# Performance work log

Measured on AMD Instinct MI355X. Metric: run time of the kernel, lower is better.

## Reference

```python
import jax, jax.numpy as jnp
import numpy as np
import math

EPS = 1e-5

def _ln(x, g, b):
    m = jnp.mean(x, axis=-1, keepdims=True)
    v = jnp.mean((x - m) ** 2, axis=-1, keepdims=True)
    return (x - m) * jax.lax.rsqrt(v + EPS) * g + b

def _heads(t, H):
    B, T, C = t.shape
    return t.reshape(B, T, H, C // H).transpose(0, 2, 1, 3)  # [B,H,T,D]

def _merge(t):
    B, H, T, D = t.shape
    return t.transpose(0, 2, 1, 3).reshape(B, T, H * D)

def _self_attn(x, w, b, pw, pb, H):
    B, T, C = x.shape
    q, k, v = jnp.split(x @ w + b, 3, axis=-1)
    q, k, v = _heads(q, H), _heads(k, H), _heads(v, H)
    D = C // H
    att = jnp.einsum('bhqd,bhkd->bhqk', q, k) * (1.0 / math.sqrt(D))
    causal = jnp.tril(jnp.ones((T, T), bool))
    att = jnp.where(causal[None, None], att, jnp.float32(-jnp.inf))
    att = jax.nn.softmax(att, axis=-1)
    out = _merge(jnp.einsum('bhqk,bhkd->bhqd', att, v))
    return out @ pw + pb

def _cross_attn(enc, dec, w, b, pw, pb, H):
    B, Td, C = dec.shape
    q_dec = jnp.split(dec @ w + b, 3, axis=-1)[0]
    _, k_enc, v_enc = jnp.split(enc @ w + b, 3, axis=-1)
    q = _heads(q_dec, H); k = _heads(k_enc, H); v = _heads(v_enc, H)
    D = C // H
    att = jnp.einsum('bhqd,bhkd->bhqk', q, k) * (1.0 / math.sqrt(D))
    att = jax.nn.softmax(att, axis=-1)
    out = _merge(jnp.einsum('bhqk,bhkd->bhqd', att, v))
    return out @ pw + pb

def _block(x, encoder_embd,
           ln1_g, ln1_b, ln2_g, ln2_b, ln3_g, ln3_b,
           attn_w, attn_b, aproj_w, aproj_b,
           ca_w, ca_b, caproj_w, caproj_b,
           fc_w, fc_b, mproj_w, mproj_b,
           down_w, down_b, up_w, up_b, H=16):
    x = x + _self_attn(_ln(x, ln1_g, ln1_b), attn_w, attn_b, aproj_w, aproj_b, H)
    x = x + _cross_attn(encoder_embd, _ln(x, ln2_g, ln2_b), ca_w, ca_b, caproj_w, caproj_b, H)
    h = jax.nn.gelu(_ln(x, ln3_g, ln3_b) @ fc_w + fc_b, approximate=True) @ mproj_w + mproj_b
    adapt = jax.nn.gelu(h @ down_w + down_b, approximate=True) @ up_w + up_b + h  # Adapter residual
    return x + adapt


def setup_inputs() -> dict:
    key = jax.random.key(0)
    ks = jax.random.split(key, 12)
    B, T, Te, C, H = 4, 1024, 257, 1024, 16
    s = 0.02
    f32 = jnp.float32
    return {
        'x': jax.random.normal(ks[0], (B, T, C), f32),
        'encoder_embd': jax.random.normal(ks[1], (B, Te, C), f32),
        'prefix_embd': jnp.zeros((B, 1, C), f32),
        'ln1_g': jnp.ones((C,), f32), 'ln1_b': jnp.zeros((C,), f32),
        'ln2_g': jnp.ones((C,), f32), 'ln2_b': jnp.zeros((C,), f32),
        'ln3_g': jnp.ones((C,), f32), 'ln3_b': jnp.zeros((C,), f32),
        'attn_w': jax.random.normal(ks[2], (C, 3 * C), f32) * s,
        'attn_b': jnp.zeros((3 * C,), f32),
        'aproj_w': jax.random.normal(ks[3], (C, C), f32) * s,
        'aproj_b': jnp.zeros((C,), f32),
        'ca_w': jax.random.normal(ks[4], (C, 3 * C), f32) * s,
        'ca_b': jnp.zeros((3 * C,), f32),
        'caproj_w': jax.random.normal(ks[5], (C, C), f32) * s,
        'caproj_b': jnp.zeros((C,), f32),
        'fc_w': jax.random.normal(ks[6], (C, 4 * C), f32) * s,
        'fc_b': jnp.zeros((4 * C,), f32),
        'mproj_w': jax.random.normal(ks[7], (4 * C, C), f32) * s,
        'mproj_b': jnp.zeros((C,), f32),
        'down_w': jax.random.normal(ks[8], (C, C // 4), f32) * s,
        'down_b': jnp.zeros((C // 4,), f32),
        'up_w': jax.random.normal(ks[9], (C // 4, C), f32) * s,
        'up_b': jnp.zeros((C,), f32),
    }


def reference(x, encoder_embd, prefix_embd,
              ln1_g, ln1_b, ln2_g, ln2_b, ln3_g, ln3_b,
              attn_w, attn_b, aproj_w, aproj_b,
              ca_w, ca_b, caproj_w, caproj_b,
              fc_w, fc_b, mproj_w, mproj_b,
              down_w, down_b, up_w, up_b):
    # prefix_embd unused (peft='adapter')
    return _block(x, encoder_embd,
                  ln1_g, ln1_b, ln2_g, ln2_b, ln3_g, ln3_b,
                  attn_w, attn_b, aproj_w, aproj_b,
                  ca_w, ca_b, caproj_w, caproj_b,
                  fc_w, fc_b, mproj_w, mproj_b,
                  down_w, down_b, up_w, up_b)
```

## Files before the change

### kernel.cpp

```cpp
#include <hip/hip_runtime.h>

typedef __attribute__((ext_vector_type(8))) short short8v;
typedef __attribute__((ext_vector_type(8))) unsigned short ushort8v;
typedef __attribute__((ext_vector_type(4))) unsigned short ushort4v;
typedef __attribute__((ext_vector_type(4))) float f32x4;

__device__ __forceinline__ unsigned short f2b(float f) {
  unsigned int u = __float_as_uint(f);
  unsigned int r = (u + 0x7FFFu + ((u >> 16) & 1u)) >> 16;
  return (unsigned short)r;
}
__device__ __forceinline__ float b2f(unsigned short h) {
  return __uint_as_float(((unsigned int)h) << 16);
}
__device__ __forceinline__ float gelu_f(float x) {
  float z = 0.7978845608028654f * (x + 0.044715f * x * x * x);
  float e = __expf(2.0f * z);
  float t = 1.0f - 2.0f / (e + 1.0f);
  return 0.5f * x * (1.0f + t);
}
__device__ __forceinline__ void gload16(const void* g, void* l) {
  __builtin_amdgcn_global_load_lds((const __attribute__((address_space(1))) unsigned int*)g,
                                   (__attribute__((address_space(3))) unsigned int*)l,
                                   16, 0, 0);
}
__device__ __forceinline__ int xcd_swz(int wgid, int nwg) {
  int q = nwg >> 3, r = nwg & 7;
  int xcd = wgid & 7, idx = wgid >> 3;
  return (xcd < r ? xcd * (q + 1) : r * (q + 1) + (xcd - r) * q) + idx;
}

__global__ __launch_bounds__(256) void k_wprep(
    const float* aw, unsigned short* awt,
    const float* apw, unsigned short* apwt,
    const float* cw, unsigned short* cwt,
    const float* cpw, unsigned short* cpwt,
    const float* fw, unsigned short* fwt,
    const float* mw, unsigned short* mwt,
    const float* dw, unsigned short* dwt,
    const float* uw, unsigned short* uwt,
    const float* enc, unsigned short* encb) {
  __shared__ float tile[64][65];
  int bid = blockIdx.x, t = threadIdx.x;
  const float* w; unsigned short* wt; int K, N, gx, l;
  if      (bid < 768)  { w = aw;  wt = awt;  K = 1024; N = 3072; gx = 48; l = bid; }
  else if (bid < 1024) { w = apw; wt = apwt; K = 1024; N = 1024; gx = 16; l = bid - 768; }
  else if (bid < 1792) { w = cw;  wt = cwt;  K = 1024; N = 3072; gx = 48; l = bid - 1024; }
  else if (bid < 2048) { w = cpw; wt = cpwt; K = 1024; N = 1024; gx = 16; l = bid - 1792; }
  else if (bid < 3072) { w = fw;  wt = fwt;  K = 1024; N = 4096; gx = 64; l = bid - 2048; }
  else if (bid < 4096) { w = mw;  wt = mwt;  K = 4096; N = 1024; gx = 16; l = bid - 3072; }
  else if (bid < 4160) { w = dw;  wt = dwt;  K = 1024; N = 256;  gx = 4;  l = bid - 4096; }
  else if (bid < 4224) { w = uw;  wt = uwt;  K = 256;  N = 1024; gx = 16; l = bid - 4160; }
  else {
    size_t i = ((size_t)(bid - 4224) * 256 + t) * 4;
    f32x4 v = *(const f32x4*)&enc[i];
    ushort4v o;
#pragma unroll
    for (int j = 0; j < 4; ++j) o[j] = f2b(v[j]);
    *(ushort4v*)&encb[i] = o;
    return;
  }
  int bx = l % gx, by = l / gx;
  int tn = bx * 64, tk = by * 64;
  int c = t & 63, r0 = t >> 6;
#pragma unroll
  for (int p = 0; p < 16; ++p) {
    int r = r0 + p * 4;
    tile[r][c] = w[(size_t)(tk + r) * N + tn + c];
  }
  __syncthreads();
#pragma unroll
  for (int p = 0; p < 16; ++p) {
    int r = r0 + p * 4;
    wt[(size_t)(tn + r) * K + tk + c] = f2b(tile[c][r]);
  }
}

__global__ __launch_bounds__(256) void k_ln(const float* __restrict__ in,
                                            const float* __restrict__ g,
                                            const float* __restrict__ b,
                                            unsigned short* __restrict__ out) {
  int row = blockIdx.x;
  const float* x = in + (size_t)row * 1024;
  int t = threadIdx.x;
  float v0 = x[t], v1 = x[t + 256], v2 = x[t + 512], v3 = x[t + 768];
  float s = v0 + v1 + v2 + v3;
  float s2 = v0 * v0 + v1 * v1 + v2 * v2 + v3 * v3;
#pragma unroll
  for (int m = 1; m < 64; m <<= 1) { s += __shfl_xor(s, m); s2 += __shfl_xor(s2, m); }
  __shared__ float rs[4], rs2[4];
  int w = t >> 6;
  if ((t & 63) == 0) { rs[w] = s; rs2[w] = s2; }
  __syncthreads();
  s = rs[0] + rs[1] + rs[2] + rs[3];
  s2 = rs2[0] + rs2[1] + rs2[2] + rs2[3];
  float mean = s * (1.0f / 1024.0f);
  float var = s2 * (1.0f / 1024.0f) - mean * mean;
  float rinv = rsqrtf(var + 1e-5f);
  unsigned short* o = out + (size_t)row * 1024;
  o[t]       = f2b((v0 - mean) * rinv * g[t]       + b[t]);
  o[t + 256] = f2b((v1 - mean) * rinv * g[t + 256] + b[t + 256]);
  o[t + 512] = f2b((v2 - mean) * rinv * g[t + 512] + b[t + 512]);
  o[t + 768] = f2b((v3 - mean) * rinv * g[t + 768] + b[t + 768]);
}

template <bool GELU, bool WF32, bool WBF16, int NRES, bool RES1B>
__global__ __launch_bounds__(256) void k_gemm(
    const unsigned short* __restrict__ A, int lda,
    const unsigned short* __restrict__ W, int ldw,
    const float* __restrict__ bias,
    const float* __restrict__ res1, const unsigned short* __restrict__ res1b,
    const float* __restrict__ res2,
    float* __restrict__ outF, unsigned short* __restrict__ outB,
    int M, int N, int K, int nbx) {
  __shared__ unsigned short lds[16384];
  const int t = threadIdx.x;
  const int swz = xcd_swz(blockIdx.x, gridDim.x);
  const int tileM = (swz / nbx) * 128, tileN = (swz % nbx) * 128;
  const int lane = t & 63, w = t >> 6;
  const int wm = (w >> 1) * 64, wn = (w & 1) * 64;
  const int lr16 = lane & 15, kc4 = lane >> 4;

  const int row1 = t >> 2, row2 = (t >> 2) + 64, cs = t & 3;
  const int c1 = (cs ^ ((row1 >> 1) & 3)) * 8;
  const int c2 = (cs ^ ((row2 >> 1) & 3)) * 8;
  int gr1 = tileM + row1; if (gr1 >= M) gr1 = M - 1;
  int gr2 = tileM + row2; if (gr2 >= M) gr2 = M - 1;
  const unsigned short* a1 = A + (size_t)gr1 * lda + c1;
  const unsigned short* a2 = A + (size_t)gr2 * lda + c2;
  const unsigned short* w1 = W + (size_t)(tileN + row1) * ldw + c1;
  const unsigned short* w2 = W + (size_t)(tileN + row2) * ldw + c2;

  f32x4 acc[4][4];
#pragma unroll
  for (int i = 0; i < 4; ++i)
#pragma unroll
    for (int j = 0; j < 4; ++j) acc[i][j] = f32x4{0.f, 0.f, 0.f, 0.f};

  const int nsteps = K >> 5;
  for (int ks = 0; ks < nsteps; ++ks) {
    const int koff = ks << 5;
    gload16(a1 + koff, &lds[t * 8]);
    gload16(a2 + koff, &lds[2048 + t * 8]);
    gload16(w1 + koff, &lds[8192 + t * 8]);
    gload16(w2 + koff, &lds[10240 + t * 8]);
    __syncthreads();
    short8v af[4], bfr[4];
#pragma unroll
    for (int i = 0; i < 4; ++i) {
      int r = wm + i * 16 + lr16;
      af[i] = *(const short8v*)&lds[r * 32 + (kc4 ^ ((r >> 1) & 3)) * 8];
    }
#pragma unroll
    for (int j = 0; j < 4; ++j) {
      int r = wn + j * 16 + lr16;
      bfr[j] = *(const short8v*)&lds[8192 + r * 32 + (kc4 ^ ((r >> 1) & 3)) * 8];
    }
#pragma unroll
    for (int i = 0; i < 4; ++i)
#pragma unroll
      for (int j = 0; j < 4; ++j)
        acc[i][j] = __builtin_amdgcn_mfma_f32_16x16x32_bf16(af[i], bfr[j], acc[i][j], 0, 0, 0);
    __syncthreads();
  }

#pragma unroll
  for (int mi = 0; mi < 4; ++mi) {
#pragma unroll
    for (int n = 0; n < 4; ++n) {
      int col = tileN + wn + n * 16 + lr16;
      float bv = bias[col];
#pragma unroll
      for (int qi = 0; qi < 4; ++qi) {
        int row = tileM + wm + mi * 16 + kc4 * 4 + qi;
        if (row < M) {
          float v = acc[mi][n][qi] + bv;
          if (GELU) v = gelu_f(v);
          size_t o = (size_t)row * N + col;
          if (NRES >= 1) v += RES1B ? b2f(res1b[o]) : res1[o];
          if (NRES >= 2) v += res2[o];
          if (WF32) outF[o] = v;
          if (WBF16) outB[o] = f2b(v);
        }
      }
    }
  }
}

__global__ __launch_bounds__(256) void k_vtrans(const unsigned short* __restrict__ src,
                                                int src_stride, int src_off, int TB,
                                                unsigned short* __restrict__ dst, int dst_tstride) {
  __shared__ unsigned short tile[64][72];
  int tb = blockIdx.x, bh = blockIdx.y;
  int b = bh >> 4, h = bh & 15;
  int t = threadIdx.x;
  int r = t >> 2, c0 = (t & 3) * 16;
  int tok = tb * 64 + r; if (tok >= TB) tok = TB - 1;
  const unsigned short* s = src + (size_t)(b * TB + tok) * src_stride + src_off + h * 64 + c0;
  *(ushort8v*)&tile[r][c0] = *(const ushort8v*)s;
  *(ushort8v*)&tile[r][c0 + 8] = *(const ushort8v*)(s + 8);
  __syncthreads();
  unsigned short tmp[16];
#pragma unroll
  for (int j = 0; j < 16; ++j) tmp[j] = tile[c0 + j][r];
  unsigned short* dp = dst + ((size_t)bh * 64 + r) * dst_tstride + tb * 64 + c0;
  *(ushort8v*)dp = *(const ushort8v*)&tmp[0];
  *(ushort8v*)(dp + 8) = *(const ushort8v*)&tmp[8];
}

template <bool CAUSAL>
__global__ __launch_bounds__(256) void k_attn(
    const unsigned short* __restrict__ Qb, int q_stride,
    const unsigned short* __restrict__ Kb, int k_stride, int k_off, int TKR,
    const unsigned short* __restrict__ Vt, int vt_tstride,
    unsigned short* __restrict__ out, int Tk) {
  __shared__ unsigned short Kl[64 * 72];
  __shared__ unsigned short Vl[64 * 72];
  __shared__ unsigned short Pl[4][16 * 72];
  const int swz = xcd_swz(blockIdx.x, gridDim.x);
  int qb = swz & 15, bh = swz >> 4;
  int b = bh >> 4, h = bh & 15;
  int t = threadIdx.x, lane = t & 63, w = t >> 6;
  int g = lane >> 4, lc = lane & 15;

  int qrow_g = qb * 64 + w * 16 + lc;
  const unsigned short* qp = Qb + (size_t)(b * 1024 + qrow_g) * q_stride + h * 64 + g * 8;
  short8v aq0 = *(const short8v*)qp;
  short8v aq1 = *(const short8v*)(qp + 32);

  f32x4 o[4];
  float m_[4], l_[4];
#pragma unroll
  for (int dt = 0; dt < 4; ++dt) o[dt] = f32x4{0.f, 0.f, 0.f, 0.f};
#pragma unroll
  for (int r = 0; r < 4; ++r) { m_[r] = -3.0e38f; l_[r] = 0.0f; }

  int srow = t >> 2;
  int sc = (t & 3) * 16;
  int ntiles = CAUSAL ? (qb + 1) : ((Tk + 63) >> 6);

  for (int kt = 0; kt < ntiles; ++kt) {
    __syncthreads();
    {
      int kg = kt * 64 + srow;
      if (!CAUSAL && kg >= Tk) kg = Tk - 1;
      const unsigned short* ks = Kb + (size_t)(b * TKR + kg) * k_stride + k_off + h * 64 + sc;
      *(ushort8v*)&Kl[srow * 72 + sc]     = *(const ushort8v*)ks;
      *(ushort8v*)&Kl[srow * 72 + sc + 8] = *(const ushort8v*)(ks + 8);
      const unsigned short* vs = Vt + ((size_t)bh * 64 + srow) * vt_tstride + kt * 64 + sc;
      *(ushort8v*)&Vl[srow * 72 + sc]     = *(const ushort8v*)vs;
      *(ushort8v*)&Vl[srow * 72 + sc + 8] = *(const ushort8v*)(vs + 8);
    }
    __syncthreads();

    f32x4 s[4];
#pragma unroll
    for (int jt = 0; jt < 4; ++jt) {
      short8v bk0 = *(const short8v*)&Kl[(jt * 16 + lc) * 72 + g * 8];
      short8v bk1 = *(const short8v*)&Kl[(jt * 16 + lc) * 72 + g * 8 + 32];
      f32x4 acc = f32x4{0.f, 0.f, 0.f, 0.f};
      acc = __builtin_amdgcn_mfma_f32_16x16x32_bf16(aq0, bk0, acc, 0, 0, 0);
      acc = __builtin_amdgcn_mfma_f32_16x16x32_bf16(aq1, bk1, acc, 0, 0, 0);
      s[jt] = acc;
    }
#pragma unroll
    for (int jt = 0; jt < 4; ++jt)
#pragma unroll
      for (int r = 0; r < 4; ++r) {
        float sv = s[jt][r] * 0.125f;
        bool masked = CAUSAL ? (kt == qb && (jt * 16 + lc) > (w * 16 + g * 4 + r))
                             : (kt * 64 + jt * 16 + lc >= Tk);
        s[jt][r] = masked ? -3.0e38f : sv;
      }
    float f[4];
#pragma unroll
    for (int r = 0; r < 4; ++r) {
      float mx = fmaxf(fmaxf(s[0][r], s[1][r]), fmaxf(s[2][r], s[3][r]));
      mx = fmaxf(mx, __shfl_xor(mx, 1));
      mx = fmaxf(mx, __shfl_xor(mx, 2));
      mx = fmaxf(mx, __shfl_xor(mx, 4));
      mx = fmaxf(mx, __shfl_xor(mx, 8));
      float mnew = fmaxf(m_[r], mx);
      f[r] = __expf(m_[r] - mnew);
      m_[r] = mnew;
      float rsum = 0.0f;
#pragma unroll
      for (int jt = 0; jt < 4; ++jt) {
        float p = __expf(s[jt][r] - mnew);
        s[jt][r] = p;
        rsum += p;
      }
      rsum += __shfl_xor(rsum, 1);
      rsum += __shfl_xor(rsum, 2);
      rsum += __shfl_xor(rsum, 4);
      rsum += __shfl_xor(rsum, 8);
      l_[r] = l_[r] * f[r] + rsum;
    }
#pragma unroll
    for (int dt = 0; dt < 4; ++dt)
#pragma unroll
      for (int r = 0; r < 4; ++r) o[dt][r] *= f[r];
#pragma unroll
    for (int jt = 0; jt < 4; ++jt)
#pragma unroll
      for (int r = 0; r < 4; ++r)
        Pl[w][(g * 4 + r) * 72 + jt * 16 + lc] = f2b(s[jt][r]);
    short8v ap0 = *(const short8v*)&Pl[w][lc * 72 + g * 8];
    short8v ap1 = *(const short8v*)&Pl[w][lc * 72 + g * 8 + 32];
#pragma unroll
    for (int dt = 0; dt < 4; ++dt) {
      short8v bv0 = *(const short8v*)&Vl[(dt * 16 + lc) * 72 + g * 8];
      short8v bv1 = *(const short8v*)&Vl[(dt * 16 + lc) * 72 + g * 8 + 32];
      o[dt] = __builtin_amdgcn_mfma_f32_16x16x32_bf16(ap0, bv0, o[dt], 0, 0, 0);
      o[dt] = __builtin_amdgcn_mfma_f32_16x16x32_bf16(ap1, bv1, o[dt], 0, 0, 0);
    }
  }
  size_t orow = (size_t)(b * 1024 + qb * 64 + w * 16) * 1024 + h * 64;
#pragma unroll
  for (int r = 0; r < 4; ++r) {
    float inv = 1.0f / l_[r];
#pragma unroll
    for (int dt = 0; dt < 4; ++dt)
      out[orow + (size_t)(g * 4 + r) * 1024 + dt * 16 + lc] = f2b(o[dt][r] * inv);
  }
}

extern "C" void kernel_launch(void* const* d_in, const int* in_sizes, int n_in,
                              void* d_out, int out_size, void* d_ws, size_t ws_size,
                              hipStream_t stream) {
  (void)in_sizes; (void)n_in; (void)out_size; (void)ws_size;
  const float* x       = (const float*)d_in[0];
  const float* enc     = (const float*)d_in[1];
  const float* ln1_g   = (const float*)d_in[3];
  const float* ln1_b   = (const float*)d_in[4];
  const float* ln2_g   = (const float*)d_in[5];
  const float* ln2_b   = (const float*)d_in[6];
  const float* ln3_g   = (const float*)d_in[7];
  const float* ln3_b   = (const float*)d_in[8];
  const float* attn_w  = (const float*)d_in[9];
  const float* attn_b  = (const float*)d_in[10];
  const float* aproj_w = (const float*)d_in[11];
  const float* aproj_b = (const float*)d_in[12];
  const float* ca_w    = (const float*)d_in[13];
  const float* ca_b    = (const float*)d_in[14];
  const float* caproj_w= (const float*)d_in[15];
  const float* caproj_b= (const float*)d_in[16];
  const float* fc_w    = (const float*)d_in[17];
  const float* fc_b    = (const float*)d_in[18];
  const float* mproj_w = (const float*)d_in[19];
  const float* mproj_b = (const float*)d_in[20];
  const float* down_w  = (const float*)d_in[21];
  const float* down_b  = (const float*)d_in[22];
  const float* up_w    = (const float*)d_in[23];
  const float* up_b    = (const float*)d_in[24];
  float* out = (float*)d_out;
  char* ws = (char*)d_ws;

  const size_t O_WATTN = 0, O_WAPROJ = 6291456, O_WCA = 8388608, O_WCAPROJ = 14680064,
               O_WFC = 16777216, O_WMPROJ = 25165824, O_WDOWN = 33554432, O_WUP = 34078720,
               O_ENC = 34603008, O_LN = 36708352, O_BIG = 45096960,
               O_XRES = 78651392, O_ATTN = 112205824;

  unsigned short* wt_attn   = (unsigned short*)(ws + O_WATTN);
  unsigned short* wt_aproj  = (unsigned short*)(ws + O_WAPROJ);
  unsigned short* wt_ca     = (unsigned short*)(ws + O_WCA);
  unsigned short* wt_caproj = (unsigned short*)(ws + O_WCAPROJ);
  unsigned short* wt_fc     = (unsigned short*)(ws + O_WFC);
  unsigned short* wt_mproj  = (unsigned short*)(ws + O_WMPROJ);
  unsigned short* wt_down   = (unsigned short*)(ws + O_WDOWN);
  unsigned short* wt_up     = (unsigned short*)(ws + O_WUP);
  unsigned short* encbf     = (unsigned short*)(ws + O_ENC);
  unsigned short* lnout     = (unsigned short*)(ws + O_LN);
  unsigned short* hbf       = (unsigned short*)(ws + O_LN);
  unsigned short* qkvb      = (unsigned short*)(ws + O_BIG);
  unsigned short* vt_self   = (unsigned short*)(ws + O_BIG + 25165824);
  unsigned short* q2b       = (unsigned short*)(ws + O_BIG);
  unsigned short* kvb       = (unsigned short*)(ws + O_BIG + 8388608);
  unsigned short* vt_cross  = (unsigned short*)(ws + O_BIG + 12599296);
  unsigned short* caout     = (unsigned short*)(ws + O_BIG + 15220736);
  unsigned short* fcout     = (unsigned short*)(ws + O_BIG);
  float*          xres      = (float*)(ws + O_XRES);
  unsigned short* attnout   = (unsigned short*)(ws + O_ATTN);
  unsigned short* dmid      = (unsigned short*)(ws + O_ATTN);

  dim3 blk(256);

  k_wprep<<<dim3(5252), blk, 0, stream>>>(
      attn_w, wt_attn, aproj_w, wt_aproj, ca_w, wt_ca, caproj_w, wt_caproj,
      fc_w, wt_fc, mproj_w, wt_mproj, down_w, wt_down, up_w, wt_up, enc, encbf);

  k_ln<<<dim3(4096), blk, 0, stream>>>(x, ln1_g, ln1_b, lnout);
  k_gemm<false, false, true, 0, false><<<dim3(768), blk, 0, stream>>>(
      lnout, 1024, wt_attn, 1024, attn_b, nullptr, nullptr, nullptr, nullptr, qkvb,
      4096, 3072, 1024, 24);
  k_vtrans<<<dim3(16, 64), blk, 0, stream>>>(qkvb, 3072, 2048, 1024, vt_self, 1024);
  k_attn<true><<<dim3(1024), blk, 0, stream>>>(
      qkvb, 3072, qkvb, 3072, 1024, 1024, vt_self, 1024, attnout, 1024);
  k_gemm<false, true, false, 1, false><<<dim3(256), blk, 0, stream>>>(
      attnout, 1024, wt_aproj, 1024, aproj_b, x, nullptr, nullptr, xres, nullptr,
      4096, 1024, 1024, 8);

  k_ln<<<dim3(4096), blk, 0, stream>>>(xres, ln2_g, ln2_b, lnout);
  k_gemm<false, false, true, 0, false><<<dim3(256), blk, 0, stream>>>(
      lnout, 1024, wt_ca, 1024, ca_b, nullptr, nullptr, nullptr, nullptr, q2b,
      4096, 1024, 1024, 8);
  k_gemm<false, false, true, 0, false><<<dim3(144), blk, 0, stream>>>(
      encbf, 1024, wt_ca + (size_t)1024 * 1024, 1024, ca_b + 1024, nullptr, nullptr,
      nullptr, nullptr, kvb, 1028, 2048, 1024, 16);
  k_vtrans<<<dim3(5, 64), blk, 0, stream>>>(kvb, 2048, 1024, 257, vt_cross, 320);
  k_attn<false><<<dim3(1024), blk, 0, stream>>>(
      q2b, 1024, kvb, 2048, 0, 257, vt_cross, 320, caout, 257);
  k_gemm<false, true, false, 1, false><<<dim3(256), blk, 0, stream>>>(
      caout, 1024, wt_caproj, 1024, caproj_b, xres, nullptr, nullptr, xres, nullptr,
      4096, 1024, 1024, 8);

  k_ln<<<dim3(4096), blk, 0, stream>>>(xres, ln3_g, ln3_b, lnout);
  k_gemm<true, false, true, 0, false><<<dim3(1024), blk, 0, stream>>>(
      lnout, 1024, wt_fc, 1024, fc_b, nullptr, nullptr, nullptr, nullptr, fcout,
      4096, 4096, 1024, 32);
  k_gemm<false, false, true, 0, false><<<dim3(256), blk, 0, stream>>>(
      fcout, 4096, wt_mproj, 4096, mproj_b, nullptr, nullptr, nullptr, nullptr, hbf,
      4096, 1024, 4096, 8);

  k_gemm<true, false, true, 0, false><<<dim3(64), blk, 0, stream>>>(
      hbf, 1024, wt_down, 1024, down_b, nullptr, nullptr, nullptr, nullptr, dmid,
      4096, 256, 1024, 2);
  k_gemm<false, true, false, 2, true><<<dim3(256), blk, 0, stream>>>(
      dmid, 256, wt_up, 256, up_b, nullptr, hbf, xres, out, nullptr,
      4096, 1024, 256, 8);
}
```

Baseline: 510.5 us.

## Add register-prefetched double-buffered GEMMs and 256x256 tiles for QKV and FC

Replaces the single-buffered direct-to-LDS GEMM mainloop with a register-staged, double-buffered pipeline. It uses a BK=64 K-step and XOR-swizzled LDS, so the global loads for the next tile overlap the MFMA work on the current one. Adds a 512-thread 256x256-tile kernel for the QKV and FC projections to raise data reuse per block. The trade is more LDS and registers per block, fewer blocks for the large GEMMs (192/256 across the CUs), and extra VGPR pressure from the prefetch registers.

New measurement: 472.7 us. 7.4% less time.

```diff
diff --git a/kernel.cpp b/kernel.cpp
--- a/kernel.cpp
+++ b/kernel.cpp
@@ -18,11 +18,6 @@
   float e = __expf(2.0f * z);
   float t = 1.0f - 2.0f / (e + 1.0f);
   return 0.5f * x * (1.0f + t);
-}
-__device__ __forceinline__ void gload16(const void* g, void* l) {
-  __builtin_amdgcn_global_load_lds((const __attribute__((address_space(1))) unsigned int*)g,
-                                   (__attribute__((address_space(3))) unsigned int*)l,
-                                   16, 0, 0);
 }
 __device__ __forceinline__ int xcd_swz(int wgid, int nwg) {
   int q = nwg >> 3, r = nwg & 7;
@@ -104,8 +99,104 @@
   o[t + 768] = f2b((v3 - mean) * rinv * g[t + 768] + b[t + 768]);
 }
 
+template <bool GELU>
+__global__ __launch_bounds__(512, 2) void k_g256r(
+    const unsigned short* __restrict__ A, int lda,
+    const unsigned short* __restrict__ W, int ldw,
+    const float* __restrict__ bias,
+    unsigned short* __restrict__ outB, int ldo, int K, int nbx) {
+  __shared__ unsigned short lds[65536];
+  const int t = threadIdx.x;
+  const int swz = xcd_swz(blockIdx.x, gridDim.x);
+  const int tileM = (swz / nbx) * 256, tileN = (swz % nbx) * 256;
+  const int lane = t & 63, w = t >> 6;
+  const int wm = w >> 2, wn = w & 3;
+  const int lr16 = lane & 15, kc4 = lane >> 4;
+
+  const int sr = t >> 1, hb = t & 1;
+  const unsigned short* ga = A + (size_t)(tileM + sr) * lda + hb * 32;
+  const unsigned short* gw = W + (size_t)(tileN + sr) * ldw + hb * 32;
+  unsigned short* const wbA = &lds[sr * 64];
+  const int wsl[4] = {((hb * 4 + 0) ^ (sr & 7)) * 8, ((hb * 4 + 1) ^ (sr & 7)) * 8,
+                      ((hb * 4 + 2) ^ (sr & 7)) * 8, ((hb * 4 + 3) ^ (sr & 7)) * 8};
+
+  f32x4 acc[8][4];
+#pragma unroll
+  for (int i = 0; i < 8; ++i)
+#pragma unroll
+    for (int j = 0; j < 4; ++j) acc[i][j] = f32x4{0.f, 0.f, 0.f, 0.f};
+
+  const int nt = K >> 6;
+  ushort8v ra[4], rb[4];
+
+#define LOADT(T)                                              \
+  do {                                                        \
+    int ko = (T) << 6;                                        \
+    _Pragma("unroll") for (int j = 0; j < 4; ++j) {           \
+      ra[j] = *(const ushort8v*)(ga + ko + j * 8);            \
+      rb[j] = *(const ushort8v*)(gw + ko + j * 8);            \
+    }                                                         \
+  } while (0)
+#define WRITET(bsel)                                          \
+  do {                                                        \
+    unsigned short* dA = wbA + (bsel) * 32768;                \
+    _Pragma("unroll") for (int j = 0; j < 4; ++j) {           \
+      *(ushort8v*)(dA + wsl[j]) = ra[j];                      \
+      *(ushort8v*)(dA + 16384 + wsl[j]) = rb[j];              \
+    }                                                         \
+  } while (0)
+
+  LOADT(0);
+  WRITET(0);
+  __syncthreads();
+
+  for (int T = 0; T < nt; ++T) {
+    if (T + 1 < nt) LOADT(T + 1);
+    const int base = (T & 1) * 32768;
+#pragma unroll
+    for (int ks = 0; ks < 2; ++ks) {
+      short8v bfr[4];
+#pragma unroll
+      for (int n = 0; n < 4; ++n) {
+        int r = wn * 64 + n * 16 + lr16;
+        int sl = ((ks * 4 + kc4) ^ (r & 7)) * 8;
+        bfr[n] = *(const short8v*)&lds[base + 16384 + r * 64 + sl];
+      }
+#pragma unroll
+      for (int mi = 0; mi < 8; ++mi) {
+        int r = wm * 128 + mi * 16 + lr16;
+        int sl = ((ks * 4 + kc4) ^ (r & 7)) * 8;
+        short8v af = *(const short8v*)&lds[base + r * 64 + sl];
+#pragma unroll
+        for (int n = 0; n < 4; ++n)
+          acc[mi][n] = __builtin_amdgcn_mfma_f32_16x16x32_bf16(af, bfr[n], acc[mi][n], 0, 0, 0);
+      }
+    }
+    if (T + 1 < nt) WRITET((T + 1) & 1);
+    __syncthreads();
+  }
+#undef LOADT
+#undef WRITET
+
+#pragma unroll
+  for (int mi = 0; mi < 8; ++mi) {
+#pragma unroll
+    for (int n = 0; n < 4; ++n) {
+      int col = tileN + wn * 64 + n * 16 + lr16;
+      float bv = bias[col];
+#pragma unroll
+      for (int qi = 0; qi < 4; ++qi) {
+        int row = tileM + wm * 128 + mi * 16 + kc4 * 4 + qi;
+        float v = acc[mi][n][qi] + bv;
+        if (GELU) v = gelu_f(v);
+        outB[(size_t)row * ldo + col] = f2b(v);
+      }
+    }
+  }
+}
+
 template <bool GELU, bool WF32, bool WBF16, int NRES, bool RES1B>
-__global__ __launch_bounds__(256) void k_gemm(
+__global__ __launch_bounds__(256, 2) void k_g128r(
     const unsigned short* __restrict__ A, int lda,
     const unsigned short* __restrict__ W, int ldw,
     const float* __restrict__ bias,
@@ -113,7 +204,7 @@
     const float* __restrict__ res2,
     float* __restrict__ outF, unsigned short* __restrict__ outB,
     int M, int N, int K, int nbx) {
-  __shared__ unsigned short lds[16384];
+  __shared__ unsigned short lds[32768];
   const int t = threadIdx.x;
   const int swz = xcd_swz(blockIdx.x, gridDim.x);
   const int tileM = (swz / nbx) * 128, tileN = (swz % nbx) * 128;
@@ -121,15 +212,13 @@
   const int wm = (w >> 1) * 64, wn = (w & 1) * 64;
   const int lr16 = lane & 15, kc4 = lane >> 4;
 
-  const int row1 = t >> 2, row2 = (t >> 2) + 64, cs = t & 3;
-  const int c1 = (cs ^ ((row1 >> 1) & 3)) * 8;
-  const int c2 = (cs ^ ((row2 >> 1) & 3)) * 8;
-  int gr1 = tileM + row1; if (gr1 >= M) gr1 = M - 1;
-  int gr2 = tileM + row2; if (gr2 >= M) gr2 = M - 1;
-  const unsigned short* a1 = A + (size_t)gr1 * lda + c1;
-  const unsigned short* a2 = A + (size_t)gr2 * lda + c2;
-  const unsigned short* w1 = W + (size_t)(tileN + row1) * ldw + c1;
-  const unsigned short* w2 = W + (size_t)(tileN + row2) * ldw + c2;
+  const int sr = t >> 1, hb = t & 1;
+  int gr = tileM + sr; if (gr >= M) gr = M - 1;
+  const unsigned short* ga = A + (size_t)gr * lda + hb * 32;
+  const unsigned short* gw = W + (size_t)(tileN + sr) * ldw + hb * 32;
+  unsigned short* const wbA = &lds[sr * 64];
+  const int wsl[4] = {((hb * 4 + 0) ^ (sr & 7)) * 8, ((hb * 4 + 1) ^ (sr & 7)) * 8,
+                      ((hb * 4 + 2) ^ (sr & 7)) * 8, ((hb * 4 + 3) ^ (sr & 7)) * 8};
 
   f32x4 acc[4][4];
 #pragma unroll
@@ -137,32 +226,57 @@
 #pragma unroll
     for (int j = 0; j < 4; ++j) acc[i][j] = f32x4{0.f, 0.f, 0.f, 0.f};
 
-  const int nsteps = K >> 5;
-  for (int ks = 0; ks < nsteps; ++ks) {
-    const int koff = ks << 5;
-    gload16(a1 + koff, &lds[t * 8]);
-    gload16(a2 + koff, &lds[2048 + t * 8]);
-    gload16(w1 + koff, &lds[8192 + t * 8]);
-    gload16(w2 + koff, &lds[10240 + t * 8]);
+  const int nt = K >> 6;
+  ushort8v ra[4], rb[4];
+
+#define LOADT(T)                                              \
+  do {                                                        \
+    int ko = (T) << 6;                                        \
+    _Pragma("unroll") for (int j = 0; j < 4; ++j) {           \
+      ra[j] = *(const ushort8v*)(ga + ko + j * 8);            \
+      rb[j] = *(const ushort8v*)(gw + ko + j * 8);            \
+    }                                                         \
+  } while (0)
+#define WRITET(bsel)                                          \
+  do {                                                        \
+    unsigned short* dA = wbA + (bsel) * 16384;                \
+    _Pragma("unroll") for (int j = 0; j < 4; ++j) {           \
+      *(ushort8v*)(dA + wsl[j]) = ra[j];                      \
+      *(ushort8v*)(dA + 8192 + wsl[j]) = rb[j];               \
+    }                                                         \
+  } while (0)
+
+  LOADT(0);
+  WRITET(0);
+  __syncthreads();
+
+  for (int T = 0; T < nt; ++T) {
+    if (T + 1 < nt) LOADT(T + 1);
+    const int base = (T & 1) * 16384;
+#pragma unroll
+    for (int ks = 0; ks < 2; ++ks) {
+      short8v bfr[4];
+#pragma unroll
+      for (int n = 0; n < 4; ++n) {
+        int r = wn + n * 16 + lr16;
+        int sl = ((ks * 4 + kc4) ^ (r & 7)) * 8;
+        bfr[n] = *(const short8v*)&lds[base + 8192 + r * 64 + sl];
+      }
+#pragma unroll
+      for (int mi = 0; mi < 4; ++mi) {
+        int r = wm + mi * 16 + lr16;
+        int sl = ((ks * 4 + kc4) ^ (r & 7)) * 8;
+        short8v af = *(const short8v*)&lds[base + r * 64 + sl];
+#pragma unroll
+        for (int n = 0; n < 4; ++n)
+          acc[mi][n] = __builtin_amdgcn_mfma_f32_16x16x32_bf16(af, bfr[n], acc[mi][n], 0, 0, 0);
+      }
+    }
+    if (T + 1 < nt) WRITET((T + 1) & 1);
     __syncthreads();
-    short8v af[4], bfr[4];
-#pragma unroll
-    for (int i = 0; i < 4; ++i) {
-      int r = wm + i * 16 + lr16;
-      af[i] = *(const short8v*)&lds[r * 32 + (kc4 ^ ((r >> 1) & 3)) * 8];
-    }
-#pragma unroll
-    for (int j = 0; j < 4; ++j) {
-      int r = wn + j * 16 + lr16;
-      bfr[j] = *(const short8v*)&lds[8192 + r * 32 + (kc4 ^ ((r >> 1) & 3)) * 8];
-    }
-#pragma unroll
-    for (int i = 0; i < 4; ++i)
-#pragma unroll
-      for (int j = 0; j < 4; ++j)
-        acc[i][j] = __builtin_amdgcn_mfma_f32_16x16x32_bf16(af[i], bfr[j], acc[i][j], 0, 0, 0);
-    __syncthreads();
-  }
+  }
+#undef LOADT
+#undef WRITET
 
 #pragma unroll
   for (int mi = 0; mi < 4; ++mi) {
@@ -384,48 +498,47 @@
   unsigned short* dmid      = (unsigned short*)(ws + O_ATTN);
 
   dim3 blk(256);
+  dim3 blk5(512);
 
   k_wprep<<<dim3(5252), blk, 0, stream>>>(
       attn_w, wt_attn, aproj_w, wt_aproj, ca_w, wt_ca, caproj_w, wt_caproj,
       fc_w, wt_fc, mproj_w, wt_mproj, down_w, wt_down, up_w, wt_up, enc, encbf);
 
   k_ln<<<dim3(4096), blk, 0, stream>>>(x, ln1_g, ln1_b, lnout);
-  k_gemm<false, false, true, 0, false><<<dim3(768), blk, 0, stream>>>(
-      lnout, 1024, wt_attn, 1024, attn_b, nullptr, nullptr, nullptr, nullptr, qkvb,
-      4096, 3072, 1024, 24);
+  k_g256r<false><<<dim3(192), blk5, 0, stream>>>(
+      lnout, 1024, wt_attn, 1024, attn_b, qkvb, 3072, 1024, 12);
   k_vtrans<<<dim3(16, 64), blk, 0, stream>>>(qkvb, 3072, 2048, 1024, vt_self, 1024);
   k_attn<true><<<dim3(1024), blk, 0, stream>>>(
       qkvb, 3072, qkvb, 3072, 1024, 1024, vt_self, 1024, attnout, 1024);
-  k_gemm<false, true, false, 1, false><<<dim3(256), blk, 0, stream>>>(
+  k_g128r<false, true, false, 1, false><<<dim3(256), blk, 0, stream>>>(
       attnout, 1024, wt_aproj, 1024, aproj_b, x, nullptr, nullptr, xres, nullptr,
       4096, 1024, 1024, 8);
 
   k_ln<<<dim3(4096), blk, 0, stream>>>(xres, ln2_g, ln2_b, lnout);
-  k_gemm<false, false, true, 0, false><<<dim3(256), blk, 0, stream>>>(
+  k_g128r<false, false, true, 0, false><<<dim3(256), blk, 0, stream>>>(
       lnout, 1024, wt_ca, 1024, ca_b, nullptr, nullptr, nullptr, nullptr, q2b,
       4096, 1024, 1024, 8);
-  k_gemm<false, false, true, 0, false><<<dim3(144), blk, 0, stream>>>(
+  k_g128r<false, false, true, 0, false><<<dim3(144), blk, 0, stream>>>(
       encbf, 1024, wt_ca + (size_t)1024 * 1024, 1024, ca_b + 1024, nullptr, nullptr,
       nullptr, nullptr, kvb, 1028, 2048, 1024, 16);
   k_vtrans<<<dim3(5, 64), blk, 0, stream>>>(kvb, 2048, 1024, 257, vt_cross, 320);
   k_attn<false><<<dim3(1024), blk, 0, stream>>>(
       q2b, 1024, kvb, 2048, 0, 257, vt_cross, 320, caout, 257);
-  k_gemm<false, true, false, 1, false><<<dim3(256), blk, 0, stream>>>(
+  k_g128r<false, true, false, 1, false><<<dim3(256), blk, 0, stream>>>(
       caout, 1024, wt_caproj, 1024, caproj_b, xres, nullptr, nullptr, xres, nullptr,
       4096, 1024, 1024, 8);
 
   k_ln<<<dim3(4096), blk, 0, stream>>>(xres, ln3_g, ln3_b, lnout);
-  k_gemm<true, false, true, 0, false><<<dim3(1024), blk, 0, stream>>>(
-      lnout, 1024, wt_fc, 1024, fc_b, nullptr, nullptr, nullptr, nullptr, fcout,
-      4096, 4096, 1024, 32);
-  k_gemm<false, false, true, 0, false><<<dim3(256), blk, 0, stream>>>(
+  k_g256r<true><<<dim3(256), blk5, 0, stream>>>(
+      lnout, 1024, wt_fc, 1024, fc_b, fcout, 4096, 1024, 16);
+  k_g128r<false, false, true, 0, false><<<dim3(256), blk, 0, stream>>>(
       fcout, 4096, wt_mproj, 4096, mproj_b, nullptr, nullptr, nullptr, nullptr, hbf,
       4096, 1024, 4096, 8);
 
-  k_gemm<true, false, true, 0, false><<<dim3(64), blk, 0, stream>>>(
+  k_g128r<true, false, true, 0, false><<<dim3(64), blk, 0, stream>>>(
       hbf, 1024, wt_down, 1024, down_b, nullptr, nullptr, nullptr, nullptr, dmid,
       4096, 256, 1024, 2);
-  k_gemm<false, true, false, 2, true><<<dim3(256), blk, 0, stream>>>(
+  k_g128r<false, true, false, 2, true><<<dim3(256), blk, 0, stream>>>(
       dmid, 256, wt_up, 256, up_b, nullptr, hbf, xres, out, nullptr,
       4096, 1024, 256, 8);
 }
```

## Double-buffer GEMM K-loop with register prefetch and 64-wide K tiles

Applied to the files above, without the earlier changes.

Replaces the direct global-to-LDS load GEMM, which synchronised twice per 32-wide K step, with a double-buffered pipeline. Each step loads the next 64-wide K tile into registers while MFMAs run on the current LDS buffer, then writes the staged registers into the alternate buffer. The change doubles LDS use to 64 KB, adds a new XOR swizzle for 64-wide rows, and sets a launch bound hint of two blocks per CU. It costs more registers for the staged fragments, and the larger LDS footprint may limit occupancy.

New measurement: 456.2 us. -10.6%, faster.

```diff
diff --git a/kernel.cpp b/kernel.cpp
--- a/kernel.cpp
+++ b/kernel.cpp
@@ -18,11 +18,6 @@
   float e = __expf(2.0f * z);
   float t = 1.0f - 2.0f / (e + 1.0f);
   return 0.5f * x * (1.0f + t);
-}
-__device__ __forceinline__ void gload16(const void* g, void* l) {
-  __builtin_amdgcn_global_load_lds((const __attribute__((address_space(1))) unsigned int*)g,
-                                   (__attribute__((address_space(3))) unsigned int*)l,
-                                   16, 0, 0);
 }
 __device__ __forceinline__ int xcd_swz(int wgid, int nwg) {
   int q = nwg >> 3, r = nwg & 7;
@@ -105,7 +100,7 @@
 }
 
 template <bool GELU, bool WF32, bool WBF16, int NRES, bool RES1B>
-__global__ __launch_bounds__(256) void k_gemm(
+__global__ __launch_bounds__(256, 2) void k_g128r(
     const unsigned short* __restrict__ A, int lda,
     const unsigned short* __restrict__ W, int ldw,
     const float* __restrict__ bias,
@@ -113,7 +108,7 @@
     const float* __restrict__ res2,
     float* __restrict__ outF, unsigned short* __restrict__ outB,
     int M, int N, int K, int nbx) {
-  __shared__ unsigned short lds[16384];
+  __shared__ unsigned short lds[32768];
   const int t = threadIdx.x;
   const int swz = xcd_swz(blockIdx.x, gridDim.x);
   const int tileM = (swz / nbx) * 128, tileN = (swz % nbx) * 128;
@@ -121,15 +116,13 @@
   const int wm = (w >> 1) * 64, wn = (w & 1) * 64;
   const int lr16 = lane & 15, kc4 = lane >> 4;
 
-  const int row1 = t >> 2, row2 = (t >> 2) + 64, cs = t & 3;
-  const int c1 = (cs ^ ((row1 >> 1) & 3)) * 8;
-  const int c2 = (cs ^ ((row2 >> 1) & 3)) * 8;
-  int gr1 = tileM + row1; if (gr1 >= M) gr1 = M - 1;
-  int gr2 = tileM + row2; if (gr2 >= M) gr2 = M - 1;
-  const unsigned short* a1 = A + (size_t)gr1 * lda + c1;
-  const unsigned short* a2 = A + (size_t)gr2 * lda + c2;
-  const unsigned short* w1 = W + (size_t)(tileN + row1) * ldw + c1;
-  const unsigned short* w2 = W + (size_t)(tileN + row2) * ldw + c2;
+  const int sr = t >> 1, hb = t & 1;
+  int gr = tileM + sr; if (gr >= M) gr = M - 1;
+  const unsigned short* ga = A + (size_t)gr * lda + hb * 32;
+  const unsigned short* gw = W + (size_t)(tileN + sr) * ldw + hb * 32;
+  unsigned short* const wbA = &lds[sr * 64];
+  const int wsl[4] = {((hb * 4 + 0) ^ (sr & 7)) * 8, ((hb * 4 + 1) ^ (sr & 7)) * 8,
+                      ((hb * 4 + 2) ^ (sr & 7)) * 8, ((hb * 4 + 3) ^ (sr & 7)) * 8};
 
   f32x4 acc[4][4];
 #pragma unroll
@@ -137,32 +130,66 @@
 #pragma unroll
     for (int j = 0; j < 4; ++j) acc[i][j] = f32x4{0.f, 0.f, 0.f, 0.f};
 
-  const int nsteps = K >> 5;
-  for (int ks = 0; ks < nsteps; ++ks) {
-    const int koff = ks << 5;
-    gload16(a1 + koff, &lds[t * 8]);
-    gload16(a2 + koff, &lds[2048 + t * 8]);
-    gload16(w1 + koff, &lds[8192 + t * 8]);
-    gload16(w2 + koff, &lds[10240 + t * 8]);
+  const int nt = K >> 6;
+  ushort8v raE[4], rbE[4], raO[4], rbO[4];
+
+#define LOADT(T, ra, rb)                                      \
+  do {                                                        \
+    int ko = (T) << 6;                                        \
+    _Pragma("unroll") for (int j = 0; j < 4; ++j) {           \
+      ra[j] = *(const ushort8v*)(ga + ko + j * 8);            \
+      rb[j] = *(const ushort8v*)(gw + ko + j * 8);            \
+    }                                                         \
+  } while (0)
+#define WRITET(ra, rb, bsel)                                  \
+  do {                                                        \
+    unsigned short* dA = wbA + (bsel) * 16384;                \
+    _Pragma("unroll") for (int j = 0; j < 4; ++j) {           \
+      *(ushort8v*)(dA + wsl[j]) = ra[j];                      \
+      *(ushort8v*)(dA + 8192 + wsl[j]) = rb[j];               \
+    }                                                         \
+  } while (0)
+#define COMPUTE(bsel)                                                           \
+  do {                                                                          \
+    const int base = (bsel) * 16384;                                            \
+    _Pragma("unroll") for (int ks = 0; ks < 2; ++ks) {                          \
+      short8v bfr[4];                                                           \
+      _Pragma("unroll") for (int n = 0; n < 4; ++n) {                           \
+        int r = wn + n * 16 + lr16;                                             \
+        int sl = ((ks * 4 + kc4) ^ (r & 7)) * 8;                                \
+        bfr[n] = *(const short8v*)&lds[base + 8192 + r * 64 + sl];              \
+      }                                                                         \
+      _Pragma("unroll") for (int mi = 0; mi < 4; ++mi) {                        \
+        int r = wm + mi * 16 + lr16;                                            \
+        int sl = ((ks * 4 + kc4) ^ (r & 7)) * 8;                                \
+        short8v af = *(const short8v*)&lds[base + r * 64 + sl];                 \
+        _Pragma("unroll") for (int n = 0; n < 4; ++n)                           \
+          acc[mi][n] =                                                          \
+              __builtin_amdgcn_mfma_f32_16x16x32_bf16(af, bfr[n], acc[mi][n], 0, 0, 0); \
+      }                                                                         \
+    }                                                                           \
+  } while (0)
+
+  LOADT(0, raE, rbE);
+  WRITET(raE, rbE, 0);
+  if (nt > 1) LOADT(1, raO, rbO);
+  __syncthreads();
+
+  for (int T = 0; T < nt; T += 2) {
+    if (T + 2 < nt) LOADT(T + 2, raE, rbE);
+    COMPUTE(0);
+    if (T + 1 < nt) WRITET(raO, rbO, 1);
     __syncthreads();
-    short8v af[4], bfr[4];
-#pragma unroll
-    for (int i = 0; i < 4; ++i) {
-      int r = wm + i * 16 + lr16;
-      af[i] = *(const short8v*)&lds[r * 32 + (kc4 ^ ((r >> 1) & 3)) * 8];
-    }
-#pragma unroll
-    for (int j = 0; j < 4; ++j) {
-      int r = wn + j * 16 + lr16;
-      bfr[j] = *(const short8v*)&lds[8192 + r * 32 + (kc4 ^ ((r >> 1) & 3)) * 8];
-    }
-#pragma unroll
-    for (int i = 0; i < 4; ++i)
-#pragma unroll
-      for (int j = 0; j < 4; ++j)
-        acc[i][j] = __builtin_amdgcn_mfma_f32_16x16x32_bf16(af[i], bfr[j], acc[i][j], 0, 0, 0);
-    __syncthreads();
-  }
+    if (T + 1 < nt) {
+      if (T + 3 < nt) LOADT(T + 3, raO, rbO);
+      COMPUTE(1);
+      if (T + 2 < nt) WRITET(raE, rbE, 0);
+      __syncthreads();
+    }
+  }
+#undef LOADT
+#undef WRITET
+#undef COMPUTE
 
 #pragma unroll
   for (int mi = 0; mi < 4; ++mi) {
@@ -390,42 +417,42 @@
       fc_w, wt_fc, mproj_w, wt_mproj, down_w, wt_down, up_w, wt_up, enc, encbf);
 
   k_ln<<<dim3(4096), blk, 0, stream>>>(x, ln1_g, ln1_b, lnout);
-  k_gemm<false, false, true, 0, false><<<dim3(768), blk, 0, stream>>>(
+  k_g128r<false, false, true, 0, false><<<dim3(768), blk, 0, stream>>>(
       lnout, 1024, wt_attn, 1024, attn_b, nullptr, nullptr, nullptr, nullptr, qkvb,
       4096, 3072, 1024, 24);
   k_vtrans<<<dim3(16, 64), blk, 0, stream>>>(qkvb, 3072, 2048, 1024, vt_self, 1024);
   k_attn<true><<<dim3(1024), blk, 0, stream>>>(
       qkvb, 3072, qkvb, 3072, 1024, 1024, vt_self, 1024, attnout, 1024);
-  k_gemm<false, true, false, 1, false><<<dim3(256), blk, 0, stream>>>(
+  k_g128r<false, true, false, 1, false><<<dim3(256), blk, 0, stream>>>(
       attnout, 1024, wt_aproj, 1024, aproj_b, x, nullptr, nullptr, xres, nullptr,
       4096, 1024, 1024, 8);
 
   k_ln<<<dim3(4096), blk, 0, stream>>>(xres, ln2_g, ln2_b, lnout);
-  k_gemm<false, false, true, 0, false><<<dim3(256), blk, 0, stream>>>(
+  k_g128r<false, false, true, 0, false><<<dim3(256), blk, 0, stream>>>(
       lnout, 1024, wt_ca, 1024, ca_b, nullptr, nullptr, nullptr, nullptr, q2b,
       4096, 1024, 1024, 8);
-  k_gemm<false, false, true, 0, false><<<dim3(144), blk, 0, stream>>>(
+  k_g128r<false, false, true, 0, false><<<dim3(144), blk, 0, stream>>>(
       encbf, 1024, wt_ca + (size_t)1024 * 1024, 1024, ca_b + 1024, nullptr, nullptr,
       nullptr, nullptr, kvb, 1028, 2048, 1024, 16);
   k_vtrans<<<dim3(5, 64), blk, 0, stream>>>(kvb, 2048, 1024, 257, vt_cross, 320);
   k_attn<false><<<dim3(1024), blk, 0, stream>>>(
       q2b, 1024, kvb, 2048, 0, 257, vt_cross, 320, caout, 257);
-  k_gemm<false, true, false, 1, false><<<dim3(256), blk, 0, stream>>>(
+  k_g128r<false, true, false, 1, false><<<dim3(256), blk, 0, stream>>>(
       caout, 1024, wt_caproj, 1024, caproj_b, xres, nullptr, nullptr, xres, nullptr,
       4096, 1024, 1024, 8);
 
   k_ln<<<dim3(4096), blk, 0, stream>>>(xres, ln3_g, ln3_b, lnout);
-  k_gemm<true, false, true, 0, false><<<dim3(1024), blk, 0, stream>>>(
+  k_g128r<true, false, true, 0, false><<<dim3(1024), blk, 0, stream>>>(
       lnout, 1024, wt_fc, 1024, fc_b, nullptr, nullptr, nullptr, nullptr, fcout,
       4096, 4096, 1024, 32);
-  k_gemm<false, false, true, 0, false><<<dim3(256), blk, 0, stream>>>(
+  k_g128r<false, false, true, 0, false><<<dim3(256), blk, 0, stream>>>(
       fcout, 4096, wt_mproj, 4096, mproj_b, nullptr, nullptr, nullptr, nullptr, hbf,
       4096, 1024, 4096, 8);
 
-  k_gemm<true, false, true, 0, false><<<dim3(64), blk, 0, stream>>>(
+  k_g128r<true, false, true, 0, false><<<dim3(64), blk, 0, stream>>>(
       hbf, 1024, wt_down, 1024, down_b, nullptr, nullptr, nullptr, nullptr, dmid,
       4096, 256, 1024, 2);
-  k_gemm<false, true, false, 2, true><<<dim3(256), blk, 0, stream>>>(
+  k_g128r<false, true, false, 2, true><<<dim3(256), blk, 0, stream>>>(
       dmid, 256, wt_up, 256, up_b, nullptr, hbf, xres, out, nullptr,
       4096, 1024, 256, 8);
 }
```
